# Kernel tuning notes

Measured on AMD Instinct MI355X. Metric: run time of the kernel, lower is better.

The kernel has to match this reference:

```python
import jax, jax.numpy as jnp
import numpy as np

B, C, H, W = 32, 256, 64, 64
K = 7  # kernel_size

def setup_inputs() -> dict:
    key = jax.random.key(0)
    kx, kw = jax.random.split(key)
    x = jax.random.normal(kx, (B, C, H, W), dtype=jnp.float32)
    # Conv2d(2, 1, 7, bias=False) weight: [out_ch=1, in_ch=2, 7, 7]
    w = jax.random.normal(kw, (1, 2, K, K), dtype=jnp.float32) * (1.0 / np.sqrt(2 * K * K))
    return {"x": x, "w": w}

def reference(x, w):
    # channel-wise max and mean, keepdim -> [B,1,H,W]
    max_out = jnp.max(x, axis=1, keepdims=True)
    avg_out = jnp.mean(x, axis=1, keepdims=True)
    concat = jnp.concatenate([max_out, avg_out], axis=1)  # [B,2,H,W]
    pad = K // 2
    conv = jax.lax.conv_general_dilated(
        concat, w,
        window_strides=(1, 1),
        padding=[(pad, pad), (pad, pad)],
        dimension_numbers=("NCHW", "OIHW", "NCHW"),
    )  # [B,1,H,W]
    scale = jax.nn.sigmoid(conv)
    return x * scale  # broadcast over channels
```

## Files before the change

kernel.cpp:

```cpp
#include <hip/hip_runtime.h>
#include <math.h>

constexpr int Bn  = 32;
constexpr int Cn  = 256;
constexpr int Hn  = 64;
constexpr int Wn  = 64;
constexpr int HW  = Hn * Wn;
constexpr int CHW = Cn * HW;
constexpr int HW4 = HW / 4;
constexpr int NPOS  = Bn * HW;
constexpr int NPOS4 = NPOS / 4;

__global__ __launch_bounds__(256) void reduce_k(const float* __restrict__ x,
                                                float* __restrict__ pmax,
                                                float* __restrict__ pavg) {
    __shared__ float4 smax[4][64];
    __shared__ float4 ssum[4][64];

    const int lane  = threadIdx.x & 63;
    const int chunk = threadIdx.x >> 6;
    const int pos4  = blockIdx.x * 64 + lane;
    const int b     = pos4 >> 10;
    const int sp4   = pos4 & (HW4 - 1);

    const float4* xp = (const float4*)x + (size_t)b * (CHW / 4)
                       + (size_t)(chunk * 64) * HW4 + sp4;

    float4 mx = make_float4(-INFINITY, -INFINITY, -INFINITY, -INFINITY);
    float4 sm = make_float4(0.f, 0.f, 0.f, 0.f);

    #pragma unroll 8
    for (int c = 0; c < 64; ++c) {
        float4 v = xp[(size_t)c * HW4];
        mx.x = fmaxf(mx.x, v.x); mx.y = fmaxf(mx.y, v.y);
        mx.z = fmaxf(mx.z, v.z); mx.w = fmaxf(mx.w, v.w);
        sm.x += v.x; sm.y += v.y; sm.z += v.z; sm.w += v.w;
    }

    smax[chunk][lane] = mx;
    ssum[chunk][lane] = sm;
    __syncthreads();

    if (chunk == 0) {
        float4 M = smax[0][lane];
        float4 S = ssum[0][lane];
        #pragma unroll
        for (int k = 1; k < 4; ++k) {
            float4 m2 = smax[k][lane];
            float4 s2 = ssum[k][lane];
            M.x = fmaxf(M.x, m2.x); M.y = fmaxf(M.y, m2.y);
            M.z = fmaxf(M.z, m2.z); M.w = fmaxf(M.w, m2.w);
            S.x += s2.x; S.y += s2.y; S.z += s2.z; S.w += s2.w;
        }
        const float inv = 1.0f / (float)Cn;
        float4 A = make_float4(S.x * inv, S.y * inv, S.z * inv, S.w * inv);
        ((float4*)pmax)[pos4] = M;
        ((float4*)pavg)[pos4] = A;
    }
}

__global__ __launch_bounds__(256) void conv_k(const float* __restrict__ pmax,
                                              const float* __restrict__ pavg,
                                              const float* __restrict__ w,
                                              float* __restrict__ scale) {
    __shared__ float sw[98];
    if (threadIdx.x < 98) sw[threadIdx.x] = w[threadIdx.x];
    __syncthreads();

    const int idx = blockIdx.x * blockDim.x + threadIdx.x;
    const int b   = idx >> 12;
    const int sp  = idx & 4095;
    const int h   = sp >> 6;
    const int wc  = sp & 63;

    const float* pm = pmax + b * HW;
    const float* pa = pavg + b * HW;

    float acc = 0.f;
    #pragma unroll
    for (int kh = 0; kh < 7; ++kh) {
        const int hh = h + kh - 3;
        if (hh < 0 || hh >= Hn) continue;
        #pragma unroll
        for (int kw = 0; kw < 7; ++kw) {
            const int ww = wc + kw - 3;
            if (ww < 0 || ww >= Wn) continue;
            const int o = hh * Wn + ww;
            acc += pm[o] * sw[kh * 7 + kw] + pa[o] * sw[49 + kh * 7 + kw];
        }
    }
    scale[idx] = 1.f / (1.f + expf(-acc));
}

__global__ __launch_bounds__(256) void mul_k(const float* __restrict__ x,
                                             const float* __restrict__ scale,
                                             float* __restrict__ out) {
    const long long i4 = (long long)blockIdx.x * 256 + threadIdx.x;
    const int b   = (int)(i4 >> 18);
    const int hw4 = (int)(i4 & (HW4 - 1));

    const float4 s = ((const float4*)scale)[b * HW4 + hw4];
    const float4 v = ((const float4*)x)[i4];
    float4 o;
    o.x = v.x * s.x; o.y = v.y * s.y; o.z = v.z * s.z; o.w = v.w * s.w;
    ((float4*)out)[i4] = o;
}

extern "C" void kernel_launch(void* const* d_in, const int* in_sizes, int n_in,
                              void* d_out, int out_size, void* d_ws, size_t ws_size,
                              hipStream_t stream) {
    const float* x = (const float*)d_in[0];
    const float* w = (const float*)d_in[1];
    float* out = (float*)d_out;

    float* pmax  = (float*)d_ws;
    float* pavg  = pmax + NPOS;
    float* scale = pavg + NPOS;

    reduce_k<<<NPOS4 / 64, 256, 0, stream>>>(x, pmax, pavg);

    conv_k<<<NPOS / 256, 256, 0, stream>>>(pmax, pavg, w, scale);

    mul_k<<<(Bn * CHW / 4) / 256, 256, 0, stream>>>(x, scale, out);
}
```

Before: 254.6 us.

## Fuse conv+sigmoid into the scaling pass and widen the channel reduction

Merges the 7x7 conv/sigmoid kernel and the broadcast multiply into one kernel. Each block stages a halo tile of the pooled max/avg maps in shared memory, computes four sigmoid scales per thread, then applies them to a 32-channel slice of x. This removes the scale buffer round-trip and one launch, at the cost of recomputing the conv eight times per tile (once per channel group). The reduction kernel now uses 512-thread blocks with eight waves of 32 channels each, giving fewer but larger blocks.

```diff
diff --git a/kernel.cpp b/kernel.cpp
--- a/kernel.cpp
+++ b/kernel.cpp
@@ -8,44 +8,48 @@
 constexpr int HW  = Hn * Wn;
 constexpr int CHW = Cn * HW;
 constexpr int HW4 = HW / 4;
-constexpr int NPOS  = Bn * HW;
-constexpr int NPOS4 = NPOS / 4;
+constexpr int NPOS = Bn * HW;
 
-__global__ __launch_bounds__(256) void reduce_k(const float* __restrict__ x,
+constexpr int TR  = 16;
+constexpr int HR  = TR + 6;
+constexpr int HC  = Wn + 6;
+constexpr int HCP = 72;
+
+__global__ __launch_bounds__(512) void reduce_k(const float* __restrict__ x,
                                                 float* __restrict__ pmax,
                                                 float* __restrict__ pavg) {
-    __shared__ float4 smax[4][64];
-    __shared__ float4 ssum[4][64];
+    __shared__ float4 smax[8][64];
+    __shared__ float4 ssum[8][64];
 
-    const int lane  = threadIdx.x & 63;
-    const int chunk = threadIdx.x >> 6;
-    const int pos4  = blockIdx.x * 64 + lane;
-    const int b     = pos4 >> 10;
-    const int sp4   = pos4 & (HW4 - 1);
+    const int lane = threadIdx.x & 63;
+    const int wv   = threadIdx.x >> 6;
+    const int pg   = blockIdx.x;
+    const int b    = pg >> 4;
+    const int sp4  = (pg & 15) * 64 + lane;
 
     const float4* xp = (const float4*)x + (size_t)b * (CHW / 4)
-                       + (size_t)(chunk * 64) * HW4 + sp4;
+                       + (size_t)(wv * 32) * HW4 + sp4;
 
     float4 mx = make_float4(-INFINITY, -INFINITY, -INFINITY, -INFINITY);
     float4 sm = make_float4(0.f, 0.f, 0.f, 0.f);
 
     #pragma unroll 8
-    for (int c = 0; c < 64; ++c) {
+    for (int c = 0; c < 32; ++c) {
         float4 v = xp[(size_t)c * HW4];
         mx.x = fmaxf(mx.x, v.x); mx.y = fmaxf(mx.y, v.y);
         mx.z = fmaxf(mx.z, v.z); mx.w = fmaxf(mx.w, v.w);
         sm.x += v.x; sm.y += v.y; sm.z += v.z; sm.w += v.w;
     }
 
-    smax[chunk][lane] = mx;
-    ssum[chunk][lane] = sm;
+    smax[wv][lane] = mx;
+    ssum[wv][lane] = sm;
     __syncthreads();
 
-    if (chunk == 0) {
+    if (wv == 0) {
         float4 M = smax[0][lane];
         float4 S = ssum[0][lane];
         #pragma unroll
-        for (int k = 1; k < 4; ++k) {
+        for (int k = 1; k < 8; ++k) {
             float4 m2 = smax[k][lane];
             float4 s2 = ssum[k][lane];
             M.x = fmaxf(M.x, m2.x); M.y = fmaxf(M.y, m2.y);
@@ -54,56 +58,82 @@
         }
         const float inv = 1.0f / (float)Cn;
         float4 A = make_float4(S.x * inv, S.y * inv, S.z * inv, S.w * inv);
-        ((float4*)pmax)[pos4] = M;
-        ((float4*)pavg)[pos4] = A;
+        const int gpos4 = b * HW4 + sp4;
+        ((float4*)pmax)[gpos4] = M;
+        ((float4*)pavg)[gpos4] = A;
     }
 }
 
-__global__ __launch_bounds__(256) void conv_k(const float* __restrict__ pmax,
-                                              const float* __restrict__ pavg,
-                                              const float* __restrict__ w,
-                                              float* __restrict__ scale) {
+__global__ __launch_bounds__(256) void fused_k(const float* __restrict__ x,
+                                               const float* __restrict__ pmax,
+                                               const float* __restrict__ pavg,
+                                               const float* __restrict__ w,
+                                               float* __restrict__ out) {
+    __shared__ float pm[HR * HCP];
+    __shared__ float pa[HR * HCP];
     __shared__ float sw[98];
-    if (threadIdx.x < 98) sw[threadIdx.x] = w[threadIdx.x];
+
+    const int t  = threadIdx.x;
+    const int cg = blockIdx.x & 7;
+    const int rt = (blockIdx.x >> 3) & 3;
+    const int b  = blockIdx.x >> 5;
+    const int r0 = rt * TR;
+
+    if (t < 98) sw[t] = w[t];
+
+    for (int i = t; i < HR * HC; i += 256) {
+        const int r  = i / HC;
+        const int c  = i % HC;
+        const int gr = r0 - 3 + r;
+        const int gc = c - 3;
+        float vm = 0.f, va = 0.f;
+        if (gr >= 0 && gr < Hn && gc >= 0 && gc < Wn) {
+            const int o = b * HW + gr * Wn + gc;
+            vm = pmax[o];
+            va = pavg[o];
+        }
+        pm[r * HCP + c] = vm;
+        pa[r * HCP + c] = va;
+    }
     __syncthreads();
 
-    const int idx = blockIdx.x * blockDim.x + threadIdx.x;
-    const int b   = idx >> 12;
-    const int sp  = idx & 4095;
-    const int h   = sp >> 6;
-    const int wc  = sp & 63;
+    const int prow = t >> 4;
+    const int pcol = (t & 15) * 4;
 
-    const float* pm = pmax + b * HW;
-    const float* pa = pavg + b * HW;
-
-    float acc = 0.f;
+    float4 acc = make_float4(0.f, 0.f, 0.f, 0.f);
     #pragma unroll
     for (int kh = 0; kh < 7; ++kh) {
-        const int hh = h + kh - 3;
-        if (hh < 0 || hh >= Hn) continue;
+        const float* rm = &pm[(prow + kh) * HCP + pcol];
+        const float* ra = &pa[(prow + kh) * HCP + pcol];
+        float wm_[10], wa_[10];
+        #pragma unroll
+        for (int i2 = 0; i2 < 10; ++i2) { wm_[i2] = rm[i2]; wa_[i2] = ra[i2]; }
         #pragma unroll
         for (int kw = 0; kw < 7; ++kw) {
-            const int ww = wc + kw - 3;
-            if (ww < 0 || ww >= Wn) continue;
-            const int o = hh * Wn + ww;
-            acc += pm[o] * sw[kh * 7 + kw] + pa[o] * sw[49 + kh * 7 + kw];
+            const float cm = sw[kh * 7 + kw];
+            const float ca = sw[49 + kh * 7 + kw];
+            acc.x += wm_[kw    ] * cm + wa_[kw    ] * ca;
+            acc.y += wm_[kw + 1] * cm + wa_[kw + 1] * ca;
+            acc.z += wm_[kw + 2] * cm + wa_[kw + 2] * ca;
+            acc.w += wm_[kw + 3] * cm + wa_[kw + 3] * ca;
         }
     }
-    scale[idx] = 1.f / (1.f + expf(-acc));
-}
+    float4 s;
+    s.x = 1.f / (1.f + expf(-acc.x));
+    s.y = 1.f / (1.f + expf(-acc.y));
+    s.z = 1.f / (1.f + expf(-acc.z));
+    s.w = 1.f / (1.f + expf(-acc.w));
 
-__global__ __launch_bounds__(256) void mul_k(const float* __restrict__ x,
-                                             const float* __restrict__ scale,
-                                             float* __restrict__ out) {
-    const long long i4 = (long long)blockIdx.x * 256 + threadIdx.x;
-    const int b   = (int)(i4 >> 18);
-    const int hw4 = (int)(i4 & (HW4 - 1));
+    const size_t base4 = (size_t)(b * Cn + cg * 32) * HW4 + (size_t)r0 * 16 + t;
+    const float4* xb = (const float4*)x + base4;
+    float4*       ob = (float4*)out + base4;
 
-    const float4 s = ((const float4*)scale)[b * HW4 + hw4];
-    const float4 v = ((const float4*)x)[i4];
-    float4 o;
-    o.x = v.x * s.x; o.y = v.y * s.y; o.z = v.z * s.z; o.w = v.w * s.w;
-    ((float4*)out)[i4] = o;
+    #pragma unroll 8
+    for (int c = 0; c < 32; ++c) {
+        float4 v = xb[(size_t)c * HW4];
+        v.x *= s.x; v.y *= s.y; v.z *= s.z; v.w *= s.w;
+        ob[(size_t)c * HW4] = v;
+    }
 }
 
 extern "C" void kernel_launch(void* const* d_in, const int* in_sizes, int n_in,
@@ -113,13 +143,9 @@
     const float* w = (const float*)d_in[1];
     float* out = (float*)d_out;
 
-    float* pmax  = (float*)d_ws;
-    float* pavg  = pmax + NPOS;
-    float* scale = pavg + NPOS;
+    float* pmax = (float*)d_ws;
+    float* pavg = pmax + NPOS;
 
-    reduce_k<<<NPOS4 / 64, 256, 0, stream>>>(x, pmax, pavg);
-
-    conv_k<<<NPOS / 256, 256, 0, stream>>>(pmax, pavg, w, scale);
-
-    mul_k<<<(Bn * CHW / 4) / 256, 256, 0, stream>>>(x, scale, out);
+    reduce_k<<<512, 512, 0, stream>>>(x, pmax, pavg);
+    fused_k<<<1024, 256, 0, stream>>>(x, pmax, pavg, w, out);
 }
```

Result: no change. 257.2 us, median of 2 (+1.0%).
